# Optimization experiments

Hardware: AMD Instinct MI355X
Metric: run time of the kernel (lower is better)

Reference implementation:

```python
import jax, jax.numpy as jnp
import numpy as np
from jax import lax

N = 163840      # total nodes
E = 2621440     # total edges (avg degree 16)
B = 4096        # number of graphs / batch
F_XD = 78       # node feature dim
L_XT = 735      # cell-line sequence length (gives 2944 after conv/pool stack)


def _params(key):
    ks = jax.random.split(key, 26)
    s = 0.05
    rn = lambda k, sh: (jax.random.normal(k, sh, jnp.float32) * s)
    p = {}
    p['W1'], p['b1'] = rn(ks[0], (78, 78)), rn(ks[1], (78,))
    p['W2'], p['b2'] = rn(ks[2], (78, 156)), rn(ks[3], (156,))
    p['W3'], p['b3'] = rn(ks[4], (156, 312)), rn(ks[5], (312,))
    p['Wg1'], p['bg1'] = rn(ks[6], (312, 1024)), rn(ks[7], (1024,))
    p['Wg2'], p['bg2'] = rn(ks[8], (1024, 128)), rn(ks[9], (128,))
    p['k1'], p['kb1'] = rn(ks[10], (32, 1, 8)), rn(ks[11], (32,))
    p['k2'], p['kb2'] = rn(ks[12], (64, 32, 8)), rn(ks[13], (64,))
    p['k3'], p['kb3'] = rn(ks[14], (128, 64, 8)), rn(ks[15], (128,))
    p['Wxt'], p['bxt'] = rn(ks[16], (2944, 128)), rn(ks[17], (128,))
    p['Wf1'], p['bf1'] = rn(ks[18], (256, 1024)), rn(ks[19], (1024,))
    p['Wf2'], p['bf2'] = rn(ks[20], (1024, 128)), rn(ks[21], (128,))
    p['Wo'], p['bo'] = rn(ks[22], (128, 1)), rn(ks[23], (1,))
    return p


def setup_inputs() -> dict:
    key = jax.random.key(0)
    k0, k1, k2, kp = jax.random.split(key, 4)
    inp = {
        'x': jax.random.normal(k0, (N, F_XD), jnp.float32),
        'edge_index': jax.random.randint(k1, (2, E), 0, N),
        'batch': jnp.arange(N) // (N // B),  # contiguous graph ids, 40 nodes/graph
        'xo': jax.random.normal(k2, (B, 1, L_XT), jnp.float32),
    }
    inp.update(_params(kp))
    return inp


def _forward(x, xo, W1, b1, W2, b2, W3, b3, Wg1, bg1, Wg2, bg2,
             k1, kb1, k2, kb2, k3, kb3, Wxt, bxt, Wf1, bf1, Wf2, bf2, Wo, bo,
             edge_index, batch):
    src, dst = edge_index[0], edge_index[1]
    # GCN symmetric norm with self-loops: deg = in-degree + 1
    deg = jax.ops.segment_sum(jnp.ones(src.shape[0], x.dtype), dst, num_segments=N) + 1.0
    dinv = lax.rsqrt(deg)
    enorm = (dinv[src] * dinv[dst])[:, None]     # [E,1]
    selfn = (dinv * dinv)[:, None]               # [N,1]

    def gcn(h, W, b):
        h = h @ W
        agg = jax.ops.segment_sum(h[src] * enorm, dst, num_segments=N)
        return agg + h * selfn + b

    h = jax.nn.relu(gcn(x, W1, b1))
    h = jax.nn.relu(gcn(h, W2, b2))
    h = jax.nn.relu(gcn(h, W3, b3))
    g = jax.ops.segment_max(h, batch, num_segments=B)   # global max pool -> [B,312]
    g = jax.nn.relu(g @ Wg1 + bg1)
    g = g @ Wg2 + bg2                                   # [B,128] (dropout = eval no-op)

    def conv1d(v, w, b):
        y = lax.conv_general_dilated(v, w, (1,), 'VALID',
                                     dimension_numbers=('NCH', 'OIH', 'NCH'))
        return y + b[None, :, None]

    def pool3(v):
        return lax.reduce_window(v, -jnp.inf, lax.max, (1, 1, 3), (1, 1, 3), 'VALID')

    t = pool3(jax.nn.relu(conv1d(xo, k1, kb1)))   # [B,32,242]
    t = pool3(jax.nn.relu(conv1d(t, k2, kb2)))    # [B,64,78]
    t = pool3(jax.nn.relu(conv1d(t, k3, kb3)))    # [B,128,23]
    t = t.reshape(B, -1) @ Wxt + bxt              # [B,128]

    c = jnp.concatenate([g, t], axis=1)           # [B,256]
    c = jax.nn.relu(c @ Wf1 + bf1)
    c = jax.nn.relu(c @ Wf2 + bf2)
    return c @ Wo + bo                            # [B,1]


def reference(x, edge_index, batch, xo, W1, b1, W2, b2, W3, b3, Wg1, bg1,
              Wg2, bg2, k1, kb1, k2, kb2, k3, kb3, Wxt, bxt, Wf1, bf1,
              Wf2, bf2, Wo, bo):
    return _forward(x, xo, W1, b1, W2, b2, W3, b3, Wg1, bg1, Wg2, bg2,
                    k1, kb1, k2, kb2, k3, kb3, Wxt, bxt, Wf1, bf1, Wf2, bf2,
                    Wo, bo, edge_index, batch)
```

## Files before the change

### kernel.cpp

```cpp
#include <hip/hip_runtime.h>
#include <hip/hip_bf16.h>

#define N_NODES 163840
#define N_EDGES 2621440
#define NB      4096

typedef __hip_bfloat16 bf16;
typedef __attribute__((ext_vector_type(8))) short short8;
typedef __attribute__((ext_vector_type(4))) float floatx4;

__device__ inline float tofloat(float v) { return v; }
__device__ inline float tofloat(bf16 v) { return __bfloat162float(v); }
__device__ inline void storev(float* p, float v) { *p = v; }
__device__ inline void storev(bf16* p, float v) { *p = __float2bfloat16(v); }
__device__ inline float s2f(short s) {
  union { unsigned u; float f; } cv;
  cv.u = ((unsigned)(unsigned short)s) << 16;
  return cv.f;
}
__device__ inline short f2s(float f) {
  bf16 b = __float2bfloat16(f);
  return *(short*)&b;
}


__global__ __launch_bounds__(256) void zero_kernel(int* __restrict__ p) {
  p[blockIdx.x * 256 + threadIdx.x] = 0;
}

__global__ __launch_bounds__(256) void count_kernel(const int* __restrict__ ei,
                                                    int* __restrict__ indeg) {
  int e = blockIdx.x * 256 + threadIdx.x;
  if (e < N_EDGES) atomicAdd(&indeg[ei[N_EDGES + e]], 1);
}

__global__ __launch_bounds__(256) void scan1_kernel(const int* __restrict__ indeg,
                                                    int* __restrict__ rowstart,
                                                    int* __restrict__ bsums,
                                                    float* __restrict__ dinv) {
  __shared__ int s[256];
  int tid = threadIdx.x;
  int i = blockIdx.x * 256 + tid;
  int v = indeg[i];
  dinv[i] = rsqrtf((float)v + 1.0f);
  s[tid] = v;
  __syncthreads();
  for (int off = 1; off < 256; off <<= 1) {
    int x = (tid >= off) ? s[tid - off] : 0;
    __syncthreads();
    s[tid] += x;
    __syncthreads();
  }
  rowstart[i] = s[tid] - v;
  if (tid == 255) bsums[blockIdx.x] = s[255];
}

__global__ void scan2_kernel(const int* __restrict__ bsums, int* __restrict__ boffs,
                             int* __restrict__ rowstart) {
  if (threadIdx.x == 0 && blockIdx.x == 0) {
    int run = 0;
    for (int i = 0; i < 640; i++) { boffs[i] = run; run += bsums[i]; }
    rowstart[N_NODES] = run;
  }
}

__global__ __launch_bounds__(256) void scan3_kernel(int* __restrict__ rowstart,
                                                    int* __restrict__ cursor,
                                                    const int* __restrict__ boffs) {
  int i = blockIdx.x * 256 + threadIdx.x;
  int v = rowstart[i] + boffs[blockIdx.x];
  rowstart[i] = v;
  cursor[i] = v;
}

__global__ __launch_bounds__(256) void scatter_kernel(const int* __restrict__ ei,
                                                      int* __restrict__ cursor,
                                                      int* __restrict__ csr_src) {
  int e = blockIdx.x * 256 + threadIdx.x;
  int lo = blockIdx.y * (N_NODES / 8);
  int hi = lo + (N_NODES / 8);
  if (e < N_EDGES) {
    int d = ei[N_EDGES + e];
    if (d >= lo && d < hi) {
      int pos = atomicAdd(&cursor[d], 1);
      csr_src[pos] = ei[e];
    }
  }
}

__global__ __launch_bounds__(256) void cast_scale_kernel(const float* __restrict__ x,
                                                         const float* __restrict__ dinv,
                                                         bf16* __restrict__ xb) {
  int i = blockIdx.x * 256 + threadIdx.x;
  if (i < N_NODES * 80) {
    int n = i / 80, f = i - n * 80;
    float v = (f < 78) ? x[n * 78 + f] * dinv[n] : 0.f;
    xb[i] = __float2bfloat16(v);
  }
}


__global__ __launch_bounds__(256) void agg80_kernel(const bf16* __restrict__ hs,
                                                    const float* __restrict__ dinv,
                                                    const int* __restrict__ rowstart,
                                                    const int* __restrict__ csr,
                                                    bf16* __restrict__ out) {
  int node = blockIdx.x * 4 + (threadIdx.x >> 6);
  int lane = threadIdx.x & 63;
  int grp = lane / 10;
  int sub = lane - grp * 10;
  bool active = grp < 6;
  int st = rowstart[node], en = rowstart[node + 1];
  int cnt = en - st + 1;
  float dn = dinv[node];
  float acc[8];
#pragma unroll
  for (int j = 0; j < 8; j++) acc[j] = 0.f;
  for (int e = 0; e < cnt; e += 6) {
    int ri = e + grp;
    bool valid = active && (ri < cnt);
    int cidx = st + ri;
    cidx = (cidx < en) ? cidx : 0;
    int row = (ri < cnt - 1) ? csr[cidx] : node;
    const short* rp = (const short*)hs + (size_t)row * 80 + sub * 8;
    short8 d = *(const short8*)rp;
    float m = valid ? 1.f : 0.f;
#pragma unroll
    for (int j = 0; j < 8; j++) acc[j] += m * s2f(d[j]);
  }
  short ob[8];
#pragma unroll
  for (int j = 0; j < 8; j++) {
    float v = acc[j];
    float t = 0.f;
#pragma unroll
    for (int g = 0; g < 6; g++) t += __shfl(v, sub + 10 * g);
    ob[j] = f2s(t * dn);
  }
  if (grp == 0) {
    short8 pk;
#pragma unroll
    for (int j = 0; j < 8; j++) pk[j] = ob[j];
    *(short8*)((short*)out + (size_t)node * 80 + sub * 8) = pk;
  }
}

__global__ __launch_bounds__(256) void agg192_kernel(const bf16* __restrict__ hs,
                                                     const float* __restrict__ dinv,
                                                     const int* __restrict__ rowstart,
                                                     const int* __restrict__ csr,
                                                     bf16* __restrict__ out) {
  int node = blockIdx.x * 4 + (threadIdx.x >> 6);
  int lane = threadIdx.x & 63;
  int grp = lane >> 3;
  int sub = lane & 7;
  int st = rowstart[node], en = rowstart[node + 1];
  int cnt = en - st + 1;
  float dn = dinv[node];
  float acc[3][8];
#pragma unroll
  for (int k = 0; k < 3; k++)
#pragma unroll
    for (int j = 0; j < 8; j++) acc[k][j] = 0.f;
  for (int e = 0; e < cnt; e += 8) {
    int ri = e + grp;
    bool valid = ri < cnt;
    int cidx = st + ri;
    cidx = (cidx < en) ? cidx : 0;
    int row = (ri < cnt - 1) ? csr[cidx] : node;
    const short* rp = (const short*)hs + (size_t)row * 192 + sub * 8;
    float m = valid ? 1.f : 0.f;
#pragma unroll
    for (int k = 0; k < 3; k++) {
      short8 d = *(const short8*)(rp + k * 64);
#pragma unroll
      for (int j = 0; j < 8; j++) acc[k][j] += m * s2f(d[j]);
    }
  }
#pragma unroll
  for (int k = 0; k < 3; k++) {
    short8 pk;
#pragma unroll
    for (int j = 0; j < 8; j++) {
      float v = acc[k][j];
      v += __shfl_xor(v, 8);
      v += __shfl_xor(v, 16);
      v += __shfl_xor(v, 32);
      pk[j] = f2s(v * dn);
    }
    if (grp == 0 && (k < 2 || sub < 4))
      *(short8*)((short*)out + (size_t)node * 160 + k * 64 + sub * 8) = pk;
  }
}

template <int NT, typename TC>
__global__ __launch_bounds__(256) void gemm_mfma_kernel(
    const bf16* __restrict__ A, const bf16* __restrict__ Bt,
    const float* __restrict__ bias, const float* __restrict__ rowScale,
    TC* __restrict__ C, int M, int Nc, int ncstore, int Ksteps, int lda,
    int kpad, int ldc, int coff, int doRelu) {
  int tid = threadIdx.x;
  int w = tid >> 6, lane = tid & 63;
  int quad = lane >> 4, l16 = lane & 15;
  int r0 = blockIdx.x * 64 + w * 16;
  int c0 = blockIdx.y * (NT * 16);
  floatx4 acc[NT];
#pragma unroll
  for (int t = 0; t < NT; t++) acc[t] = (floatx4){0.f, 0.f, 0.f, 0.f};
  const short* Ap = (const short*)A + (size_t)(r0 + l16) * lda + quad * 8;
  const short* Bp = (const short*)Bt + (size_t)(c0 + l16) * kpad + quad * 8;
  for (int s = 0; s < Ksteps; s++) {
    short8 a = *(const short8*)(Ap + s * 32);
#pragma unroll
    for (int t = 0; t < NT; t++) {
      short8 b = *(const short8*)(Bp + (size_t)t * 16 * kpad + s * 32);
      acc[t] = __builtin_amdgcn_mfma_f32_16x16x32_bf16(a, b, acc[t], 0, 0, 0);
    }
  }
#pragma unroll
  for (int t = 0; t < NT; t++) {
    int c = c0 + t * 16 + l16;
    if (c >= ncstore) continue;
    bool valid = c < Nc;
    float bb = (bias && valid) ? bias[c] : 0.f;
#pragma unroll
    for (int r = 0; r < 4; r++) {
      int row = r0 + quad * 4 + r;
      float v = valid ? acc[t][r] + bb : 0.f;
      if (doRelu) v = fmaxf(v, 0.f);
      if (rowScale) v *= rowScale[row];
      storev(&C[(size_t)row * ldc + coff + c], v);
    }
  }
}

__device__ inline void wtrans_one(const float* __restrict__ W, bf16* __restrict__ Bt,
                                  int K, int N, int Kpad, int idx) {
  int n = idx / Kpad, k = idx - n * Kpad;
  float v = (k < K && n < N) ? W[(size_t)k * N + n] : 0.f;
  Bt[idx] = __float2bfloat16(v);
}
template <int CI, int NCO>
__device__ inline void wprep_one(const float* __restrict__ kw, bf16* __restrict__ Wr,
                                 int idx) {
  int co = idx % NCO, k = idx / NCO;
  int dl = k / CI, ci = k % CI;
  Wr[idx] = __float2bfloat16(kw[(co * CI + ci) * 8 + dl]);
}
__global__ __launch_bounds__(256) void wprep_all_kernel(
    const float* k2, const float* k3, const float* W1, const float* W2,
    const float* W3, const float* Wg1, const float* Wg2, const float* Wxt,
    const float* Wf1, const float* Wf2, bf16* Wr2, bf16* Wr3, bf16* Btw1,
    bf16* Btw2, bf16* BtW3, bf16* Btg1, bf16* Btg2, bf16* Btxt, bf16* Btf1,
    bf16* Btf2) {
  int idx = blockIdx.x * 256 + threadIdx.x;
  if (idx < 16384) { wprep_one<32, 64>(k2, Wr2, idx); return; }
  idx -= 16384;
  if (idx < 65536) { wprep_one<64, 128>(k3, Wr3, idx); return; }
  idx -= 65536;
  if (idx < 7680) { wtrans_one(W1, Btw1, 78, 78, 96, idx); return; }
  idx -= 7680;
  if (idx < 15360) { wtrans_one(W2, Btw2, 78, 156, 96, idx); return; }
  idx -= 15360;
  if (idx < 51200) { wtrans_one(W3, BtW3, 156, 312, 160, idx); return; }
  idx -= 51200;
  if (idx < 327680) { wtrans_one(Wg1, Btg1, 312, 1024, 320, idx); return; }
  idx -= 327680;
  if (idx < 131072) { wtrans_one(Wg2, Btg2, 1024, 128, 1024, idx); return; }
  idx -= 131072;
  if (idx < 376832) {
    int o = idx / 2944, k = idx - o * 2944;
    int l = k >> 7, co = k & 127;
    Btxt[idx] = __float2bfloat16(Wxt[((size_t)(co * 23 + l)) * 128 + o]);
    return;
  }
  idx -= 376832;
  if (idx < 262144) { wtrans_one(Wf1, Btf1, 256, 1024, 256, idx); return; }
  idx -= 262144;
  if (idx < 131072) { wtrans_one(Wf2, Btf2, 1024, 128, 1024, idx); return; }
}
#define WPREP_TOTAL (16384 + 65536 + 7680 + 15360 + 51200 + 327680 + 131072 + 376832 + 262144 + 131072)

__global__ __launch_bounds__(256) void gcn3_segmax_mfma_kernel(
    const bf16* __restrict__ agg2, const bf16* __restrict__ BtW3,
    const float* __restrict__ b3, bf16* __restrict__ g) {
  __shared__ __align__(16) bf16 a_lds[160 * 168];
  int tid = threadIdx.x;
  int w = tid >> 6, lane = tid & 63;
  int quad = lane >> 4, l16 = lane & 15;
  int g0 = blockIdx.x * 4;

  short8 bfrag[5][5];
  const short* Bp = (const short*)BtW3 + (size_t)(w * 80 + l16) * 160 + quad * 8;
#pragma unroll
  for (int nt = 0; nt < 5; nt++)
#pragma unroll
    for (int ks = 0; ks < 5; ks++)
      bfrag[nt][ks] = *(const short8*)(Bp + (size_t)nt * 16 * 160 + ks * 32);

  const bf16* src = agg2 + (size_t)g0 * 40 * 160;
  for (int i = tid; i < 160 * 160 / 8; i += 256) {
    int flat = i * 8;
    int row = flat / 160, k = flat - row * 160;
    *(short8*)&a_lds[row * 168 + k] = *(const short8*)&src[flat];
  }
  __syncthreads();

  float gmax[5][4];
#pragma unroll
  for (int nt = 0; nt < 5; nt++)
#pragma unroll
    for (int gi = 0; gi < 4; gi++) gmax[nt][gi] = -3.0e38f;

#pragma unroll
  for (int mt = 0; mt < 10; mt++) {
    floatx4 acc[5];
#pragma unroll
    for (int nt = 0; nt < 5; nt++) acc[nt] = (floatx4){0.f, 0.f, 0.f, 0.f};
#pragma unroll
    for (int ks = 0; ks < 5; ks++) {
      short8 a = *(const short8*)&a_lds[(16 * mt + l16) * 168 + ks * 32 + quad * 8];
#pragma unroll
      for (int nt = 0; nt < 5; nt++)
        acc[nt] = __builtin_amdgcn_mfma_f32_16x16x32_bf16(a, bfrag[nt][ks], acc[nt], 0, 0, 0);
    }
    int gl = (16 * mt + quad * 4) / 40;
#pragma unroll
    for (int nt = 0; nt < 5; nt++) {
      float m4 = fmaxf(fmaxf(acc[nt][0], acc[nt][1]), fmaxf(acc[nt][2], acc[nt][3]));
#pragma unroll
      for (int gi = 0; gi < 4; gi++)
        if (gl == gi) gmax[nt][gi] = fmaxf(gmax[nt][gi], m4);
    }
  }

#pragma unroll
  for (int nt = 0; nt < 5; nt++) {
#pragma unroll
    for (int gi = 0; gi < 4; gi++) {
      float v = gmax[nt][gi];
      v = fmaxf(v, __shfl_xor(v, 16));
      v = fmaxf(v, __shfl_xor(v, 32));
      gmax[nt][gi] = v;
    }
    int c = w * 80 + nt * 16 + l16;
    float bb = (c < 312) ? b3[c] : 0.f;
    float val = fmaxf(gmax[nt][quad] + bb, 0.f);
    g[(size_t)(g0 + quad) * 320 + c] = __float2bfloat16(val);
  }
}

__global__ __launch_bounds__(256) void conv1_kernel(const float* __restrict__ xo,
                                                    const float* __restrict__ k1,
                                                    const float* __restrict__ kb1,
                                                    bf16* __restrict__ out) {
  __shared__ float xin[735];
  int b = blockIdx.x, tid = threadIdx.x;
  for (int i = tid; i < 735; i += 256) xin[i] = xo[b * 735 + i];
  int co = tid & 31;
  float wreg[8];
#pragma unroll
  for (int k = 0; k < 8; k++) wreg[k] = k1[co * 8 + k];
  float bs = kb1[co];
  __syncthreads();
  for (int idx = tid; idx < 242 * 32; idx += 256) {
    int l = idx >> 5;
    int base = l * 3;
    float a0 = bs, a1 = bs, a2 = bs;
#pragma unroll
    for (int k = 0; k < 8; k++) {
      float wv = wreg[k];
      a0 += wv * xin[base + k];
      a1 += wv * xin[base + 1 + k];
      a2 += wv * xin[base + 2 + k];
    }
    out[(size_t)b * (242 * 32) + idx] =
        __float2bfloat16(fmaxf(0.f, fmaxf(a0, fmaxf(a1, a2))));
  }
}

template <int CI, int LIN, int LPAD, int MT, int LOUT, int G, int NCO>
__global__ __launch_bounds__(256) void convmfma_kernel(const bf16* __restrict__ in,
                                                       const bf16* __restrict__ Wr,
                                                       const float* __restrict__ kb,
                                                       bf16* __restrict__ outp) {
  constexpr int KSTEPS = 8 * CI / 32;
  constexpr int CIP = CI + 8;
  __shared__ __align__(16) bf16 lds_in[G * LPAD * CIP];
  __shared__ bf16 stg[4][MT * 16][16];
  int tid = threadIdx.x;
  int w = tid >> 6, lane = tid & 63;
  int quad = lane >> 4, l16 = lane & 15;
  int bg = blockIdx.x;
  int co0 = blockIdx.y * 64 + w * 16;

  short8 bfrag[KSTEPS];
#pragma unroll
  for (int s = 0; s < KSTEPS; s++) {
#pragma unroll
    for (int j = 0; j < 8; j++) {
      int k = s * 32 + quad * 8 + j;
      bfrag[s][j] = ((const short*)Wr)[k * NCO + co0 + l16];
    }
  }

  const bf16* gin = in + (size_t)bg * G * LIN * CI;
  constexpr int NELEM = G * LIN * CI;
  for (int i = tid; i < NELEM / 8; i += 256) {
    int flat = i * 8;
    int g = flat / (LIN * CI);
    int rem = flat - g * (LIN * CI);
    int row = rem / CI, ci = rem - row * CI;
    *(short8*)&lds_in[(g * LPAD + row) * CIP + ci] = *(const short8*)&gin[flat];
  }
  constexpr int PADE = G * (LPAD - LIN) * CIP;
  for (int i = tid; i < PADE / 8; i += 256) {
    int flat = i * 8;
    int g = flat / ((LPAD - LIN) * CIP);
    int rem = flat - g * ((LPAD - LIN) * CIP);
    short8 z = {0, 0, 0, 0, 0, 0, 0, 0};
    *(short8*)&lds_in[(g * LPAD + LIN) * CIP + rem] = z;
  }
  __syncthreads();

  for (int g = 0; g < G; g++) {
    const bf16* base = &lds_in[g * LPAD * CIP];
#pragma unroll
    for (int mt = 0; mt < MT; mt++) {
      floatx4 acc = {0.f, 0.f, 0.f, 0.f};
      int m = mt * 16 + l16;
#pragma unroll
      for (int s = 0; s < KSTEPS; s++) {
        int kg0 = s * 32 + quad * 8;
        int dl = kg0 / CI;
        int ci0 = kg0 % CI;
        short8 a = *(const short8*)&base[(m + dl) * CIP + ci0];
        acc = __builtin_amdgcn_mfma_f32_16x16x32_bf16(a, bfrag[s], acc, 0, 0, 0);
      }
#pragma unroll
      for (int r = 0; r < 4; r++)
        stg[w][mt * 16 + quad * 4 + r][l16] = __float2bfloat16(acc[r]);
    }
    __syncthreads();
    float bias = kb[co0 + l16];
    for (int it = lane; it < LOUT * 16; it += 64) {
      int l = it >> 4;
      float v0 = __bfloat162float(stg[w][3 * l][l16]);
      float v1 = __bfloat162float(stg[w][3 * l + 1][l16]);
      float v2 = __bfloat162float(stg[w][3 * l + 2][l16]);
      float v = fmaxf(fmaxf(v0, v1), v2) + bias;
      outp[((size_t)(bg * G + g) * LOUT + l) * NCO + co0 + l16] =
          __float2bfloat16(fmaxf(v, 0.f));
    }
    __syncthreads();
  }
}

__global__ __launch_bounds__(256) void final_kernel(const float* __restrict__ f2,
                                                    const float* __restrict__ Wo,
                                                    const float* __restrict__ bo,
                                                    float* __restrict__ out) {
  int wid = (blockIdx.x * blockDim.x + threadIdx.x) >> 6;
  int lane = threadIdx.x & 63;
  if (wid >= NB) return;
  float s = f2[wid * 128 + lane] * Wo[lane] + f2[wid * 128 + 64 + lane] * Wo[64 + lane];
  for (int o = 32; o > 0; o >>= 1) s += __shfl_down(s, o);
  if (lane == 0) out[wid] = s + bo[0];
}

extern "C" void kernel_launch(void* const* d_in, const int* in_sizes, int n_in,
                              void* d_out, int out_size, void* d_ws, size_t ws_size,
                              hipStream_t stream) {
  const float* x   = (const float*)d_in[0];
  const int*   ei  = (const int*)d_in[1];
  const float* xo  = (const float*)d_in[3];
  const float* W1  = (const float*)d_in[4];  const float* b1  = (const float*)d_in[5];
  const float* W2  = (const float*)d_in[6];  const float* b2  = (const float*)d_in[7];
  const float* W3  = (const float*)d_in[8];  const float* b3  = (const float*)d_in[9];
  const float* Wg1 = (const float*)d_in[10]; const float* bg1 = (const float*)d_in[11];
  const float* Wg2 = (const float*)d_in[12]; const float* bg2 = (const float*)d_in[13];
  const float* k1  = (const float*)d_in[14]; const float* kb1 = (const float*)d_in[15];
  const float* k2  = (const float*)d_in[16]; const float* kb2 = (const float*)d_in[17];
  const float* k3  = (const float*)d_in[18]; const float* kb3 = (const float*)d_in[19];
  const float* Wxt = (const float*)d_in[20]; const float* bxt = (const float*)d_in[21];
  const float* Wf1 = (const float*)d_in[22]; const float* bf1 = (const float*)d_in[23];
  const float* Wf2 = (const float*)d_in[24]; const float* bf2 = (const float*)d_in[25];
  const float* Wo  = (const float*)d_in[26]; const float* bo  = (const float*)d_in[27];
  float* out = (float*)d_out;

  char* ws = (char*)d_ws;
  size_t off = 0;
  auto alloc = [&](size_t bytes) -> void* {
    void* p = ws + off;
    off += (bytes + 255) & ~(size_t)255;
    return p;
  };

  int*   indeg   = (int*)alloc((size_t)N_NODES * 4);
  float* dinv    = (float*)alloc((size_t)N_NODES * 4);
  int*   rowstart= (int*)alloc((size_t)(N_NODES + 1) * 4);
  int*   cursor  = (int*)alloc((size_t)N_NODES * 4);
  int*   bsums   = (int*)alloc(640 * 4);
  int*   boffs   = (int*)alloc(640 * 4);
  int*   csr     = (int*)alloc((size_t)N_EDGES * 4 + 256);
  bf16*  nb1     = (bf16*)alloc((size_t)N_NODES * 160 * 2);
  bf16*  nb2     = (bf16*)alloc((size_t)NB * 7744 * 2);
  bf16*  gb      = (bf16*)alloc((size_t)NB * 320 * 2);
  bf16*  g1b     = (bf16*)alloc((size_t)NB * 1024 * 2);
  bf16*  gtb     = (bf16*)alloc((size_t)NB * 256 * 2);
  float* f2      = (float*)alloc((size_t)NB * 128 * 4);
  bf16*  Wr2     = (bf16*)alloc((size_t)256 * 64 * 2);
  bf16*  Wr3     = (bf16*)alloc((size_t)512 * 128 * 2);
  bf16*  Btw1    = (bf16*)alloc((size_t)80 * 96 * 2);
  bf16*  Btw2    = (bf16*)alloc((size_t)160 * 96 * 2);
  bf16*  BtW3    = (bf16*)alloc((size_t)320 * 160 * 2);
  bf16*  Btg1    = (bf16*)alloc((size_t)1024 * 320 * 2);
  bf16*  Btg2    = (bf16*)alloc((size_t)128 * 1024 * 2);
  bf16*  Btxt    = (bf16*)alloc((size_t)128 * 2944 * 2);
  bf16*  Btf1    = (bf16*)alloc((size_t)1024 * 256 * 2);
  bf16*  Btf2    = (bf16*)alloc((size_t)128 * 1024 * 2);

  bf16* xb  = nb2;
  bf16* h   = nb2;
  bf16* ag  = nb1;
  bf16* c1  = nb2;
  bf16* c2  = nb1;
  bf16* c3  = nb2;
  bf16* f1b = g1b;

  wprep_all_kernel<<<(WPREP_TOTAL + 255) / 256, 256, 0, stream>>>(
      k2, k3, W1, W2, W3, Wg1, Wg2, Wxt, Wf1, Wf2, Wr2, Wr3, Btw1, Btw2, BtW3,
      Btg1, Btg2, Btxt, Btf1, Btf2);

  zero_kernel<<<N_NODES / 256, 256, 0, stream>>>(indeg);
  count_kernel<<<N_EDGES / 256, 256, 0, stream>>>(ei, indeg);
  scan1_kernel<<<640, 256, 0, stream>>>(indeg, rowstart, bsums, dinv);
  scan2_kernel<<<1, 64, 0, stream>>>(bsums, boffs, rowstart);
  scan3_kernel<<<640, 256, 0, stream>>>(rowstart, cursor, boffs);
  scatter_kernel<<<dim3(N_EDGES / 256, 8), 256, 0, stream>>>(ei, cursor, csr);

  cast_scale_kernel<<<(N_NODES * 80 + 255) / 256, 256, 0, stream>>>(x, dinv, xb);
  agg80_kernel<<<N_NODES / 4, 256, 0, stream>>>(xb, dinv, rowstart, csr, ag);
  gemm_mfma_kernel<5, bf16><<<dim3(N_NODES / 64, 1), 256, 0, stream>>>(
      ag, Btw1, b1, dinv, h, N_NODES, 78, 80, 3, 80, 96, 80, 0, 1);
  agg80_kernel<<<N_NODES / 4, 256, 0, stream>>>(h, dinv, rowstart, csr, ag);
  gemm_mfma_kernel<6, bf16><<<dim3(N_NODES / 64, 2), 256, 0, stream>>>(
      ag, Btw2, b2, dinv, h, N_NODES, 156, 192, 3, 80, 96, 192, 0, 1);
  agg192_kernel<<<N_NODES / 4, 256, 0, stream>>>(h, dinv, rowstart, csr, ag);
  gcn3_segmax_mfma_kernel<<<NB / 4, 256, 0, stream>>>(ag, BtW3, b3, gb);

  gemm_mfma_kernel<4, bf16><<<dim3(NB / 64, 16), 256, 0, stream>>>(
      gb, Btg1, bg1, nullptr, g1b, NB, 1024, 1024, 10, 320, 320, 1024, 0, 1);
  gemm_mfma_kernel<4, bf16><<<dim3(NB / 64, 2), 256, 0, stream>>>(
      g1b, Btg2, bg2, nullptr, gtb, NB, 128, 128, 32, 1024, 1024, 256, 0, 0);

  conv1_kernel<<<NB, 256, 0, stream>>>(xo, k1, kb1, c1);
  convmfma_kernel<32, 242, 248, 15, 78, 2, 64>
      <<<dim3(NB / 2, 1), 256, 0, stream>>>(c1, Wr2, kb2, c2);
  convmfma_kernel<64, 78, 88, 5, 23, 4, 128>
      <<<dim3(NB / 4, 2), 256, 0, stream>>>(c2, Wr3, kb3, c3);
  gemm_mfma_kernel<4, bf16><<<dim3(NB / 64, 2), 256, 0, stream>>>(
      c3, Btxt, bxt, nullptr, gtb, NB, 128, 128, 92, 2944, 2944, 256, 128, 0);

  gemm_mfma_kernel<4, bf16><<<dim3(NB / 64, 16), 256, 0, stream>>>(
      gtb, Btf1, bf1, nullptr, f1b, NB, 1024, 1024, 8, 256, 256, 1024, 0, 1);
  gemm_mfma_kernel<4, float><<<dim3(NB / 64, 2), 256, 0, stream>>>(
      f1b, Btf2, bf2, nullptr, f2, NB, 128, 128, 32, 1024, 1024, 128, 0, 1);
  final_kernel<<<NB * 64 / 256, 256, 0, stream>>>(f2, Wo, bo, out);
}
```

Baseline: 1.157 ms.

## Fuse conv1 into conv2 MFMA kernel, parallelize block scan, fold zeroing into wprep

Conv1 (with ReLU and pool) now runs directly into shared memory inside the conv2 MFMA kernel, so the [B,32,242] intermediate is never written to or read back from global memory. The single-thread serial scan over block sums becomes a 640-thread parallel scan. Zeroing of the in-degree array moves into the weight-prep kernel, removing one launch. The CSR scatter uses 4 destination partitions instead of 8, so the edge list is read fewer times, at the cost of more atomic spread per pass.

```diff
diff --git a/kernel.cpp b/kernel.cpp
--- a/kernel.cpp
+++ b/kernel.cpp
@@ -23,10 +23,6 @@
   return *(short*)&b;
 }
 
-
-__global__ __launch_bounds__(256) void zero_kernel(int* __restrict__ p) {
-  p[blockIdx.x * 256 + threadIdx.x] = 0;
-}
 
 __global__ __launch_bounds__(256) void count_kernel(const int* __restrict__ ei,
                                                     int* __restrict__ indeg) {
@@ -55,13 +51,22 @@
   if (tid == 255) bsums[blockIdx.x] = s[255];
 }
 
-__global__ void scan2_kernel(const int* __restrict__ bsums, int* __restrict__ boffs,
-                             int* __restrict__ rowstart) {
-  if (threadIdx.x == 0 && blockIdx.x == 0) {
-    int run = 0;
-    for (int i = 0; i < 640; i++) { boffs[i] = run; run += bsums[i]; }
-    rowstart[N_NODES] = run;
-  }
+__global__ __launch_bounds__(640) void scan2_kernel(const int* __restrict__ bsums,
+                                                    int* __restrict__ boffs,
+                                                    int* __restrict__ rowstart) {
+  __shared__ int s[640];
+  int tid = threadIdx.x;
+  int v = bsums[tid];
+  s[tid] = v;
+  __syncthreads();
+  for (int off = 1; off < 640; off <<= 1) {
+    int x = (tid >= off) ? s[tid - off] : 0;
+    __syncthreads();
+    s[tid] += x;
+    __syncthreads();
+  }
+  boffs[tid] = s[tid] - v;
+  if (tid == 639) rowstart[N_NODES] = s[639];
 }
 
 __global__ __launch_bounds__(256) void scan3_kernel(int* __restrict__ rowstart,
@@ -77,8 +82,8 @@
                                                       int* __restrict__ cursor,
                                                       int* __restrict__ csr_src) {
   int e = blockIdx.x * 256 + threadIdx.x;
-  int lo = blockIdx.y * (N_NODES / 8);
-  int hi = lo + (N_NODES / 8);
+  int lo = blockIdx.y * (N_NODES / 4);
+  int hi = lo + (N_NODES / 4);
   if (e < N_EDGES) {
     int d = ei[N_EDGES + e];
     if (d >= lo && d < hi) {
@@ -98,7 +103,6 @@
     xb[i] = __float2bfloat16(v);
   }
 }
-
 
 __global__ __launch_bounds__(256) void agg80_kernel(const bf16* __restrict__ hs,
                                                     const float* __restrict__ dinv,
@@ -252,8 +256,10 @@
     const float* W3, const float* Wg1, const float* Wg2, const float* Wxt,
     const float* Wf1, const float* Wf2, bf16* Wr2, bf16* Wr3, bf16* Btw1,
     bf16* Btw2, bf16* BtW3, bf16* Btg1, bf16* Btg2, bf16* Btxt, bf16* Btf1,
-    bf16* Btf2) {
+    bf16* Btf2, int* indeg) {
   int idx = blockIdx.x * 256 + threadIdx.x;
+  if (idx < N_NODES) { indeg[idx] = 0; return; }
+  idx -= N_NODES;
   if (idx < 16384) { wprep_one<32, 64>(k2, Wr2, idx); return; }
   idx -= 16384;
   if (idx < 65536) { wprep_one<64, 128>(k3, Wr3, idx); return; }
@@ -279,7 +285,7 @@
   idx -= 262144;
   if (idx < 131072) { wtrans_one(Wf2, Btf2, 1024, 128, 1024, idx); return; }
 }
-#define WPREP_TOTAL (16384 + 65536 + 7680 + 15360 + 51200 + 327680 + 131072 + 376832 + 262144 + 131072)
+#define WPREP_TOTAL (N_NODES + 16384 + 65536 + 7680 + 15360 + 51200 + 327680 + 131072 + 376832 + 262144 + 131072)
 
 __global__ __launch_bounds__(256) void gcn3_segmax_mfma_kernel(
     const bf16* __restrict__ agg2, const bf16* __restrict__ BtW3,
@@ -350,32 +356,95 @@
   }
 }
 
-__global__ __launch_bounds__(256) void conv1_kernel(const float* __restrict__ xo,
-                                                    const float* __restrict__ k1,
-                                                    const float* __restrict__ kb1,
-                                                    bf16* __restrict__ out) {
-  __shared__ float xin[735];
-  int b = blockIdx.x, tid = threadIdx.x;
-  for (int i = tid; i < 735; i += 256) xin[i] = xo[b * 735 + i];
-  int co = tid & 31;
-  float wreg[8];
-#pragma unroll
-  for (int k = 0; k < 8; k++) wreg[k] = k1[co * 8 + k];
-  float bs = kb1[co];
+__global__ __launch_bounds__(256) void conv12_kernel(const float* __restrict__ xo,
+                                                     const float* __restrict__ k1,
+                                                     const float* __restrict__ kb1,
+                                                     const bf16* __restrict__ Wr2,
+                                                     const float* __restrict__ kb2,
+                                                     bf16* __restrict__ outp) {
+  constexpr int LPAD = 248, MT = 15, LOUT = 78, G = 2, NCO = 64, CIP = 40;
+  __shared__ __align__(16) bf16 lds_in[G * LPAD * CIP];
+  __shared__ bf16 stg[4][MT * 16][16];
+  __shared__ float xo_s[G][736];
+  __shared__ float k1w[256];
+  __shared__ float kb1s[32];
+  int tid = threadIdx.x;
+  int w = tid >> 6, lane = tid & 63;
+  int quad = lane >> 4, l16 = lane & 15;
+  int bg = blockIdx.x;
+  int co0 = w * 16;
+
+  short8 bfrag[8];
+#pragma unroll
+  for (int s = 0; s < 8; s++) {
+#pragma unroll
+    for (int j = 0; j < 8; j++) {
+      int k = s * 32 + quad * 8 + j;
+      bfrag[s][j] = ((const short*)Wr2)[k * NCO + co0 + l16];
+    }
+  }
+
+  for (int i = tid; i < G * 735; i += 256)
+    xo_s[i / 735][i % 735] = xo[(size_t)(bg * G + i / 735) * 735 + i % 735];
+  k1w[tid] = k1[tid];
+  if (tid < 32) kb1s[tid] = kb1[tid];
   __syncthreads();
-  for (int idx = tid; idx < 242 * 32; idx += 256) {
-    int l = idx >> 5;
+
+  for (int idx = tid; idx < G * 242 * 32; idx += 256) {
+    int g = idx / (242 * 32);
+    int rem = idx - g * (242 * 32);
+    int l = rem >> 5, co = rem & 31;
     int base = l * 3;
+    float bs = kb1s[co];
     float a0 = bs, a1 = bs, a2 = bs;
 #pragma unroll
     for (int k = 0; k < 8; k++) {
-      float wv = wreg[k];
-      a0 += wv * xin[base + k];
-      a1 += wv * xin[base + 1 + k];
-      a2 += wv * xin[base + 2 + k];
-    }
-    out[(size_t)b * (242 * 32) + idx] =
+      float wv = k1w[co * 8 + k];
+      a0 += wv * xo_s[g][base + k];
+      a1 += wv * xo_s[g][base + 1 + k];
+      a2 += wv * xo_s[g][base + 2 + k];
+    }
+    lds_in[(g * LPAD + l) * CIP + co] =
         __float2bfloat16(fmaxf(0.f, fmaxf(a0, fmaxf(a1, a2))));
+  }
+  for (int i = tid; i < G * 6 * 32; i += 256) {
+    int g = i / (6 * 32);
+    int rem = i - g * (6 * 32);
+    int r = rem >> 5, c = rem & 31;
+    lds_in[(g * LPAD + 242 + r) * CIP + c] = __float2bfloat16(0.f);
+  }
+  __syncthreads();
+
+  for (int g = 0; g < G; g++) {
+    const bf16* base = &lds_in[g * LPAD * CIP];
+#pragma unroll
+    for (int mt = 0; mt < MT; mt++) {
+      floatx4 acc = {0.f, 0.f, 0.f, 0.f};
+      int m = mt * 16 + l16;
+#pragma unroll
+      for (int s = 0; s < 8; s++) {
+        int kg0 = s * 32 + quad * 8;
+        int dl = kg0 >> 5;
+        int ci0 = kg0 & 31;
+        short8 a = *(const short8*)&base[(m + dl) * CIP + ci0];
+        acc = __builtin_amdgcn_mfma_f32_16x16x32_bf16(a, bfrag[s], acc, 0, 0, 0);
+      }
+#pragma unroll
+      for (int r = 0; r < 4; r++)
+        stg[w][mt * 16 + quad * 4 + r][l16] = __float2bfloat16(acc[r]);
+    }
+    __syncthreads();
+    float bias = kb2[co0 + l16];
+    for (int it = lane; it < LOUT * 16; it += 64) {
+      int l = it >> 4;
+      float v0 = __bfloat162float(stg[w][3 * l][l16]);
+      float v1 = __bfloat162float(stg[w][3 * l + 1][l16]);
+      float v2 = __bfloat162float(stg[w][3 * l + 2][l16]);
+      float v = fmaxf(fmaxf(v0, v1), v2) + bias;
+      outp[((size_t)(bg * G + g) * LOUT + l) * NCO + co0 + l16] =
+          __float2bfloat16(fmaxf(v, 0.f));
+    }
+    __syncthreads();
   }
 }
 
@@ -523,21 +592,19 @@
   bf16* xb  = nb2;
   bf16* h   = nb2;
   bf16* ag  = nb1;
-  bf16* c1  = nb2;
   bf16* c2  = nb1;
   bf16* c3  = nb2;
   bf16* f1b = g1b;
 
   wprep_all_kernel<<<(WPREP_TOTAL + 255) / 256, 256, 0, stream>>>(
       k2, k3, W1, W2, W3, Wg1, Wg2, Wxt, Wf1, Wf2, Wr2, Wr3, Btw1, Btw2, BtW3,
-      Btg1, Btg2, Btxt, Btf1, Btf2);
-
-  zero_kernel<<<N_NODES / 256, 256, 0, stream>>>(indeg);
+      Btg1, Btg2, Btxt, Btf1, Btf2, indeg);
+
   count_kernel<<<N_EDGES / 256, 256, 0, stream>>>(ei, indeg);
   scan1_kernel<<<640, 256, 0, stream>>>(indeg, rowstart, bsums, dinv);
-  scan2_kernel<<<1, 64, 0, stream>>>(bsums, boffs, rowstart);
+  scan2_kernel<<<1, 640, 0, stream>>>(bsums, boffs, rowstart);
   scan3_kernel<<<640, 256, 0, stream>>>(rowstart, cursor, boffs);
-  scatter_kernel<<<dim3(N_EDGES / 256, 8), 256, 0, stream>>>(ei, cursor, csr);
+  scatter_kernel<<<dim3(N_EDGES / 256, 4), 256, 0, stream>>>(ei, cursor, csr);
 
   cast_scale_kernel<<<(N_NODES * 80 + 255) / 256, 256, 0, stream>>>(x, dinv, xb);
   agg80_kernel<<<N_NODES / 4, 256, 0, stream>>>(xb, dinv, rowstart, csr, ag);
@@ -554,9 +621,7 @@
   gemm_mfma_kernel<4, bf16><<<dim3(NB / 64, 2), 256, 0, stream>>>(
       g1b, Btg2, bg2, nullptr, gtb, NB, 128, 128, 32, 1024, 1024, 256, 0, 0);
 
-  conv1_kernel<<<NB, 256, 0, stream>>>(xo, k1, kb1, c1);
-  convmfma_kernel<32, 242, 248, 15, 78, 2, 64>
-      <<<dim3(NB / 2, 1), 256, 0, stream>>>(c1, Wr2, kb2, c2);
+  conv12_kernel<<<NB / 2, 256, 0, stream>>>(xo, k1, kb1, Wr2, kb2, c2);
   convmfma_kernel<64, 78, 88, 5, 23, 4, 128>
       <<<dim3(NB / 4, 2), 256, 0, stream>>>(c2, Wr3, kb3, c3);
   gemm_mfma_kernel<4, bf16><<<dim3(NB / 64, 2), 256, 0, stream>>>(
```

Measured after the change: 1.166 ms. About the same (+0.8%).
